# Optimization experiments

Hardware: AMD Instinct MI355X
Metric: run time of the kernel (lower is better)

The kernel has to match this reference:

```python
import jax, jax.numpy as jnp
import numpy as np

N = 10000        # nodes
E = 160000       # edges (avg degree 16)
MUL = 16         # multiplicity of each irrep in node features: '16x0e + 16x1o'
DIM_IN = 4 * MUL # 16 scalars + 16 vectors(3) = 64
DIM_SH = 4       # '1x0e + 1x1o' spherical harmonics
EMB = 18         # 2*4 (type embeds) + 10 (distance embed)
HID = 256
WNUM = 4 * MUL * MUL  # 4 tensor-product paths, 16x16 weights each


def setup_inputs() -> dict:
    key = jax.random.key(0)
    ks = jax.random.split(key, 8)
    node_features = jax.random.normal(ks[0], (N, DIM_IN), jnp.float32)
    edge_src = jax.random.randint(ks[1], (E,), 0, N, dtype=jnp.int32)
    edge_dst = jax.random.randint(ks[2], (E,), 0, N, dtype=jnp.int32)
    edge_attr = jax.random.normal(ks[3], (E, DIM_SH), jnp.float32)
    edge_embedding = jax.random.normal(ks[4], (E, EMB), jnp.float32)
    W1 = jax.random.normal(ks[5], (EMB, HID), jnp.float32) / np.sqrt(EMB)
    b1 = jnp.zeros((HID,), jnp.float32)
    W2 = jax.random.normal(ks[6], (HID, WNUM), jnp.float32) / np.sqrt(HID)
    b2 = jnp.zeros((WNUM,), jnp.float32)
    return dict(node_features=node_features, edge_attr=edge_attr,
                edge_embedding=edge_embedding, W1=W1, b1=b1, W2=W2, b2=b2,
                edge_src=edge_src, edge_dst=edge_dst)


def reference(node_features, edge_attr, edge_embedding, W1, b1, W2, b2, edge_src, edge_dst):
    # ---- edge MLP generates per-edge tensor-product weights ----
    h = jax.nn.silu(edge_embedding @ W1 + b1)          # [E, HID]
    w = (h @ W2 + b2).reshape(E, 4, MUL, MUL)          # [E, 4, 16, 16]
    w_ss, w_vv, w_sv, w_vs = w[:, 0], w[:, 1], w[:, 2], w[:, 3]

    # ---- gather source node features, split into irreps ----
    x = node_features[edge_src]                        # [E, 64]
    s = x[:, :MUL]                                     # [E, 16]   16x0e
    v = x[:, MUL:].reshape(E, MUL, 3)                  # [E, 16, 3] 16x1o
    y0 = edge_attr[:, 0]                               # [E]       1x0e sh
    y1 = edge_attr[:, 1:4]                             # [E, 3]    1x1o sh

    # ---- weighted Clebsch-Gordan tensor product (lmax=1 paths) ----
    inv_sqrt3 = np.float32(1.0 / np.sqrt(3.0))         # w3j(1,1,0), w3j(0,1,1), w3j(1,0,1)
    c_s = np.float32(np.sqrt(1.0 / (2 * MUL)))         # path norm: 2 paths, fan_in MUL each, out dim 1
    c_v = np.float32(np.sqrt(3.0 / (2 * MUL)))         # path norm: 2 paths, fan_in MUL each, out dim 3
    # 0e x 0e -> 0e  and  1o x 1o -> 0e
    out_s = c_s * (jnp.einsum('eij,e,ei->ej', w_ss, y0, s)
                   + inv_sqrt3 * jnp.einsum('eij,ea,eia->ej', w_vv, y1, v))   # [E, 16]
    # 0e x 1o -> 1o  and  1o x 0e -> 1o
    out_v = (c_v * inv_sqrt3) * (jnp.einsum('eij,ei,ea->eja', w_sv, s, y1)
                                 + jnp.einsum('eij,eia,e->eja', w_vs, v, y0))  # [E, 16, 3]

    edge_features = jnp.concatenate([out_s, out_v.reshape(E, 3 * MUL)], axis=1)  # [E, 64]

    # ---- scatter-reduce to destination nodes, normalized by sqrt(avg degree) ----
    num_neighbors = E / float(N)
    out = jax.ops.segment_sum(edge_features, edge_dst, num_segments=N)
    return out / np.float32(np.sqrt(num_neighbors))
```

## Files before the change

kernel.cpp:

```cpp
#include <hip/hip_runtime.h>
#include <math.h>


typedef __attribute__((ext_vector_type(8))) short s8v;
typedef __attribute__((ext_vector_type(4))) float f4v;
typedef unsigned short ushort_t;
typedef unsigned int uint_t;

#define NTHR 256
#define TE 64

__device__ __forceinline__ ushort_t f2bf(float x) {
    uint_t u = __float_as_uint(x);
    u += 0x7fffu + ((u >> 16) & 1u);
    return (ushort_t)(u >> 16);
}
__device__ __forceinline__ float bf2f(ushort_t v) {
    return __uint_as_float((uint_t)v << 16);
}

__global__ void prep_kernel(const float* __restrict__ W2, ushort_t* __restrict__ W2bf,
                            const int* __restrict__ edst, int* __restrict__ counts, int E) {
    if (blockIdx.x < 256) {
        int idx = blockIdx.x * 256 + threadIdx.x;
        int n  = idx & 1023;
        int k4 = (idx >> 10) << 2;
        uint_t lo = (uint_t)f2bf(W2[(size_t)(k4 + 0) * 1024 + n]) |
                    ((uint_t)f2bf(W2[(size_t)(k4 + 1) * 1024 + n]) << 16);
        uint_t hi = (uint_t)f2bf(W2[(size_t)(k4 + 2) * 1024 + n]) |
                    ((uint_t)f2bf(W2[(size_t)(k4 + 3) * 1024 + n]) << 16);
        ((uint2*)W2bf)[(n * 256 + k4) >> 2] = make_uint2(lo, hi);
    } else {
        int i = (blockIdx.x - 256) * 256 + threadIdx.x;
        if (i < E) atomicAdd(&counts[edst[i]], 1);
    }
}

__global__ __launch_bounds__(1024)
void scan_kernel(const int* __restrict__ counts, int* __restrict__ offsets, int N) {
    __shared__ int sdata[1024];
    const int t = threadIdx.x;
    const int C = (N + 1023) / 1024;
    const int lo = t * C;
    const int hi = min(lo + C, N);
    int sum = 0;
    for (int i = lo; i < hi; ++i) sum += counts[i];
    sdata[t] = sum;
    __syncthreads();
    for (int s = 1; s < 1024; s <<= 1) {
        int v = (t >= s) ? sdata[t - s] : 0;
        __syncthreads();
        sdata[t] += v;
        __syncthreads();
    }
    int run = sdata[t] - sum;
    for (int i = lo; i < hi; ++i) { offsets[i] = run; run += counts[i]; }
    if (t == 1023) offsets[N] = run;
}

__global__ __launch_bounds__(256)
void gather_kernel(const ushort_t* __restrict__ F,
                   const int* __restrict__ offsets,
                   const int* __restrict__ elist,
                   float* __restrict__ out, int N) {
    const int lane = threadIdx.x & 63;
    const int node = (blockIdx.x * 256 + threadIdx.x) >> 6;
    if (node >= N) return;
    const int base = offsets[node];
    const int end  = offsets[node + 1];
    float acc = 0.f;
    for (int j0 = base; j0 < end; j0 += 64) {
        const int rem = min(64, end - j0);
        int myeid = (lane < rem) ? elist[j0 + lane] : 0;
        int j = 0;
        for (; j + 4 <= rem; j += 4) {
            const int a0 = __shfl(myeid, j    );
            const int a1 = __shfl(myeid, j + 1);
            const int a2 = __shfl(myeid, j + 2);
            const int a3 = __shfl(myeid, j + 3);
            const float r0 = bf2f(F[(size_t)a0 * 64 + lane]);
            const float r1 = bf2f(F[(size_t)a1 * 64 + lane]);
            const float r2 = bf2f(F[(size_t)a2 * 64 + lane]);
            const float r3 = bf2f(F[(size_t)a3 * 64 + lane]);
            acc += (r0 + r1) + (r2 + r3);
        }
        for (; j < rem; ++j) {
            const int a = __shfl(myeid, j);
            acc += bf2f(F[(size_t)a * 64 + lane]);
        }
    }
    out[(size_t)node * 64 + lane] = acc;
}

__global__ __launch_bounds__(NTHR, 2)
void nequip_mfma(const float* __restrict__ nodef,
                 const float* __restrict__ eattr,
                 const float* __restrict__ eemb,
                 const float* __restrict__ W1,
                 const float* __restrict__ b1,
                 const ushort_t* __restrict__ W2bf,
                 const float* __restrict__ b2,
                 const int* __restrict__ esrc,
                 const int* __restrict__ edst,
                 const int* __restrict__ offs,
                 int* __restrict__ cursor,
                 int* __restrict__ elist,
                 ushort_t* __restrict__ F,
                 int E, float CC)
{
    __shared__ __align__(16) ushort_t sAu[TE * 256];
    __shared__ __align__(16) float sB2[1024];
    __shared__ __align__(16) float sEmb[TE * 18];
    __shared__ __align__(16) float sCss[16 * 64];
    __shared__ __align__(16) float sCvv[16 * 64];
    __shared__ __align__(16) float sCsv[16 * 64];
    __shared__ __align__(16) float sCvs[48 * 64];
    __shared__ __align__(16) float sAttrT[4 * 64];
    __shared__ __align__(16) float resSS[64 * 16];
    __shared__ __align__(16) float resSV[64 * 16];

    const int t  = threadIdx.x;
    const int e0 = blockIdx.x * TE;

    ((float4*)sB2)[t] = ((const float4*)b2)[t];
    for (int idx = t; idx < TE * 18; idx += NTHR) {
        size_t g = (size_t)e0 * 18 + idx;
        sEmb[idx] = (g < (size_t)E * 18) ? eemb[g] : 0.f;
    }
    if (t < TE) {
        int ge = e0 + t;
        float4 a = make_float4(0.f, 0.f, 0.f, 0.f);
        if (ge < E) {
            a = *(const float4*)(eattr + (size_t)ge * 4);
            const int d = edst[ge];
            const int pos = offs[d] + atomicAdd(&cursor[d], 1);
            elist[pos] = ge;
        }
        sAttrT[0 * 64 + t] = a.x; sAttrT[1 * 64 + t] = a.y;
        sAttrT[2 * 64 + t] = a.z; sAttrT[3 * 64 + t] = a.w;
    }
    {
        const int e = t >> 2, iq = t & 3;
        const int ge = e0 + e;
        const bool ok = ge < E;
        float y0 = 0.f, y1x = 0.f, y1y = 0.f, y1z = 0.f;
        int src = 0;
        if (ok) {
            float4 a = *(const float4*)(eattr + (size_t)ge * 4);
            y0 = a.x; y1x = a.y; y1y = a.z; y1z = a.w;
            src = esrc[ge];
        }
        const float* xp = nodef + (size_t)src * 64;
        float4 z = make_float4(0.f, 0.f, 0.f, 0.f);
        float4 sv = ok ? *(const float4*)(xp + iq * 4) : z;
        float4 v0 = ok ? *(const float4*)(xp + 16 + iq * 12) : z;
        float4 v1 = ok ? *(const float4*)(xp + 16 + iq * 12 + 4) : z;
        float4 v2 = ok ? *(const float4*)(xp + 16 + iq * 12 + 8) : z;
        const float K3 = CC * 0.57735026918962576f;
        float sarr[4] = { sv.x, sv.y, sv.z, sv.w };
        float varr[12] = { v0.x, v0.y, v0.z, v0.w, v1.x, v1.y, v1.z, v1.w,
                           v2.x, v2.y, v2.z, v2.w };
        #pragma unroll
        for (int j = 0; j < 4; ++j) {
            const int i = iq * 4 + j;
            const float s  = sarr[j];
            const float vx = varr[j * 3 + 0], vy = varr[j * 3 + 1], vz = varr[j * 3 + 2];
            sCss[i * 64 + e] = CC * y0 * s;
            sCvv[i * 64 + e] = K3 * (y1x * vx + y1y * vy + y1z * vz);
            sCsv[i * 64 + e] = CC * s;
            sCvs[(i * 3 + 0) * 64 + e] = CC * y0 * vx;
            sCvs[(i * 3 + 1) * 64 + e] = CC * y0 * vy;
            sCvs[(i * 3 + 2) * 64 + e] = CC * y0 * vz;
        }
    }
    __syncthreads();

    {
        const int p = t & 127;
        const int ehalf = t >> 7;
        const int n0 = 2 * p;
        float w1a[18], w1b[18];
        #pragma unroll
        for (int m = 0; m < 18; ++m) {
            float2 wv = *(const float2*)(W1 + m * 256 + n0);
            w1a[m] = wv.x; w1b[m] = wv.y;
        }
        const float2 bv = *(const float2*)(b1 + n0);
        const int kk = p >> 4;
        const int lhi = 16 * ((p >> 2) & 3);
        const int wsub = p & 3;
        uint_t* sA32 = (uint_t*)sAu;
        for (int er = 0; er < 32; ++er) {
            const int e = ehalf * 32 + er;
            float a0 = bv.x, a1 = bv.y;
            const float* ep = sEmb + e * 18;
            #pragma unroll
            for (int m = 0; m < 18; ++m) {
                const float em = ep[m];
                a0 = fmaf(em, w1a[m], a0);
                a1 = fmaf(em, w1b[m], a1);
            }
            a0 = a0 / (1.f + __expf(-a0));
            a1 = a1 / (1.f + __expf(-a1));
            const uint_t pk = (uint_t)f2bf(a0) | ((uint_t)f2bf(a1) << 16);
            const int lane_sw = ((e & 15) + lhi) ^ kk;
            sA32[(((e >> 4) * 8 + kk) * 64 + lane_sw) * 4 + wsub] = pk;
        }
    }
    __syncthreads();

    const int lane = t & 63;
    const int slab = t >> 6;
    const int jj   = lane & 15;
    const int q4   = lane >> 4;

    const ushort_t* Bl = W2bf + (size_t)jj * 256 + q4 * 8;

    float pS[4][4] = {{0.f}};
    float pV[3][4][4] = {{{0.f}}};

    if (slab < 3) {
        const float* C = (slab == 0) ? sCss : (slab == 1) ? sCvv : sCsv;
        #pragma unroll 1
        for (int g = 0; g < 8; ++g) {
            const int nb0 = slab * 256 + (2 * g) * 16;
            const int nb1 = nb0 + 16;
            f4v accA[4], accB[4];
            {
                const float bz0 = sB2[nb0 + jj];
                const float bz1 = sB2[nb1 + jj];
                #pragma unroll
                for (int mt = 0; mt < 4; ++mt) {
                    f4v zA; zA[0] = bz0; zA[1] = bz0; zA[2] = bz0; zA[3] = bz0;
                    f4v zB; zB[0] = bz1; zB[1] = bz1; zB[2] = bz1; zB[3] = bz1;
                    accA[mt] = zA; accB[mt] = zB;
                }
            }
            #pragma unroll
            for (int kk = 0; kk < 8; ++kk) {
                const s8v b0 = *(const s8v*)(Bl + (size_t)nb0 * 256 + kk * 32);
                const s8v b1 = *(const s8v*)(Bl + (size_t)nb1 * 256 + kk * 32);
                #pragma unroll
                for (int mt = 0; mt < 4; ++mt) {
                    const s8v a = *(const s8v*)(sAu + ((mt * 8 + kk) * 64 + (lane ^ kk)) * 8);
                    accA[mt] = __builtin_amdgcn_mfma_f32_16x16x32_bf16(a, b0, accA[mt], 0, 0, 0);
                    accB[mt] = __builtin_amdgcn_mfma_f32_16x16x32_bf16(a, b1, accB[mt], 0, 0, 0);
                }
            }
            const int i0 = 2 * g, i1 = 2 * g + 1;
            #pragma unroll
            for (int mt = 0; mt < 4; ++mt) {
                const int ebase = mt * 16 + q4 * 4;
                const float4 c0 = *(const float4*)(C + i0 * 64 + ebase);
                const float4 c1 = *(const float4*)(C + i1 * 64 + ebase);
                pS[mt][0] += c0.x * accA[mt][0] + c1.x * accB[mt][0];
                pS[mt][1] += c0.y * accA[mt][1] + c1.y * accB[mt][1];
                pS[mt][2] += c0.z * accA[mt][2] + c1.z * accB[mt][2];
                pS[mt][3] += c0.w * accA[mt][3] + c1.w * accB[mt][3];
            }
        }
        if (slab == 0) {
            #pragma unroll
            for (int mt = 0; mt < 4; ++mt)
                #pragma unroll
                for (int q = 0; q < 4; ++q)
                    resSS[(mt * 16 + q4 * 4 + q) * 16 + jj] = pS[mt][q];
        } else if (slab == 2) {
            #pragma unroll
            for (int mt = 0; mt < 4; ++mt)
                #pragma unroll
                for (int q = 0; q < 4; ++q)
                    resSV[(mt * 16 + q4 * 4 + q) * 16 + jj] = pS[mt][q];
        }
    } else {
        #pragma unroll
        for (int half = 0; half < 2; ++half) {
            #pragma unroll 1
            for (int g = 0; g < 8; ++g) {
                const int i0 = 2 * g, i1 = 2 * g + 1;
                const int nb0 = 3 * 256 + i0 * 16;
                const int nb1 = nb0 + 16;
                f4v acc0[2], acc1[2];
                {
                    const float bz0 = sB2[nb0 + jj];
                    const float bz1 = sB2[nb1 + jj];
                    #pragma unroll
                    for (int mt = 0; mt < 2; ++mt) {
                        f4v z0; z0[0] = bz0; z0[1] = bz0; z0[2] = bz0; z0[3] = bz0;
                        f4v z1; z1[0] = bz1; z1[1] = bz1; z1[2] = bz1; z1[3] = bz1;
                        acc0[mt] = z0; acc1[mt] = z1;
                    }
                }
                #pragma unroll
                for (int kk = 0; kk < 8; ++kk) {
                    const s8v b0 = *(const s8v*)(Bl + (size_t)nb0 * 256 + kk * 32);
                    const s8v b1 = *(const s8v*)(Bl + (size_t)nb1 * 256 + kk * 32);
                    #pragma unroll
                    for (int mt = 0; mt < 2; ++mt) {
                        const int mtg = half * 2 + mt;
                        const s8v a = *(const s8v*)(sAu + ((mtg * 8 + kk) * 64 + (lane ^ kk)) * 8);
                        acc0[mt] = __builtin_amdgcn_mfma_f32_16x16x32_bf16(a, b0, acc0[mt], 0, 0, 0);
                        acc1[mt] = __builtin_amdgcn_mfma_f32_16x16x32_bf16(a, b1, acc1[mt], 0, 0, 0);
                    }
                }
                #pragma unroll
                for (int mt = 0; mt < 2; ++mt) {
                    const int mtg = half * 2 + mt;
                    const int ebase = mtg * 16 + q4 * 4;
                    #pragma unroll
                    for (int a = 0; a < 3; ++a) {
                        const float4 c0 = *(const float4*)(sCvs + (i0 * 3 + a) * 64 + ebase);
                        const float4 c1 = *(const float4*)(sCvs + (i1 * 3 + a) * 64 + ebase);
                        pV[a][mtg][0] += c0.x * acc0[mt][0] + c1.x * acc1[mt][0];
                        pV[a][mtg][1] += c0.y * acc0[mt][1] + c1.y * acc1[mt][1];
                        pV[a][mtg][2] += c0.z * acc0[mt][2] + c1.z * acc1[mt][2];
                        pV[a][mtg][3] += c0.w * acc0[mt][3] + c1.w * acc1[mt][3];
                    }
                }
            }
        }
    }
    __syncthreads();

    if (slab == 1) {
        #pragma unroll
        for (int mt = 0; mt < 4; ++mt) {
            #pragma unroll
            for (int q = 0; q < 4; ++q) {
                const int e = mt * 16 + q4 * 4 + q;
                const int ge = e0 + e;
                if (ge < E) F[(size_t)ge * 64 + jj] = f2bf(resSS[e * 16 + jj] + pS[mt][q]);
            }
        }
    } else if (slab == 3) {
        #pragma unroll
        for (int mt = 0; mt < 4; ++mt) {
            #pragma unroll
            for (int q = 0; q < 4; ++q) {
                const int e = mt * 16 + q4 * 4 + q;
                const int ge = e0 + e;
                const float sv = resSV[e * 16 + jj];
                if (ge < E) {
                    #pragma unroll
                    for (int a = 0; a < 3; ++a)
                        F[(size_t)ge * 64 + 16 + jj * 3 + a] =
                            f2bf(fmaf(sAttrT[(1 + a) * 64 + e], sv, pV[a][mt][q]));
                }
            }
        }
    }
}

extern "C" void kernel_launch(void* const* d_in, const int* in_sizes, int n_in,
                              void* d_out, int out_size, void* d_ws, size_t ws_size,
                              hipStream_t stream)
{
    const float* node_features = (const float*)d_in[0];
    const float* edge_attr     = (const float*)d_in[1];
    const float* edge_emb      = (const float*)d_in[2];
    const float* W1            = (const float*)d_in[3];
    const float* b1            = (const float*)d_in[4];
    const float* W2            = (const float*)d_in[5];
    const float* b2            = (const float*)d_in[6];
    const int*   edge_src      = (const int*)d_in[7];
    const int*   edge_dst      = (const int*)d_in[8];
    float*       out           = (float*)d_out;

    const int E = in_sizes[7];
    const int N = out_size / 64;
    const float num_neigh = (float)E / (float)N;
    const float CC = 0.17677669529663689f / sqrtf(num_neigh);

    char* ws = (char*)d_ws;
    size_t off = 0;
    auto alloc = [&](size_t bytes) { char* p = ws + off; off = (off + bytes + 255) & ~(size_t)255; return p; };
    ushort_t* W2bf   = (ushort_t*)alloc((size_t)1024 * 256 * 2);
    int*      counts = (int*)alloc((size_t)2 * N * 4);
    int*      cursor = counts + N;
    int*      offs   = (int*)alloc((size_t)(N + 1) * 4);
    int*      elist  = (int*)alloc((size_t)E * 4);
    ushort_t* F      = (ushort_t*)alloc((size_t)E * 64 * 2);
    (void)ws_size;

    hipMemsetAsync(counts, 0, (size_t)2 * N * 4, stream);

    const int histBlocks = (E + 255) / 256;
    prep_kernel<<<256 + histBlocks, 256, 0, stream>>>(W2, W2bf, edge_dst, counts, E);
    scan_kernel<<<1, 1024, 0, stream>>>(counts, offs, N);

    const int blocks = (E + TE - 1) / TE;
    nequip_mfma<<<blocks, NTHR, 0, stream>>>(
        node_features, edge_attr, edge_emb, W1, b1, W2bf, b2,
        edge_src, edge_dst, offs, cursor, elist, F, E, CC);

    gather_kernel<<<(N + 3) / 4, 256, 0, stream>>>(F, offs, elist, out, N);
}
```

Before: 341.1 us.

## Double-buffer W2 fragment loads across groups and unify slab MFMA loops

The per-group W2 B-fragment global loads are moved into register double buffers, so the next group's fragments are prefetched while the current group's MFMAs run. The vector slab no longer runs two halves of 2 M-tiles each and instead does all 4 M-tiles in one pass, which halves its B-fragment reloads. The shared embedding rows are padded to 20 floats so the first-layer MLP can read them with float4 loads. Holding 32 s8v registers raises register pressure, which may cause spills or lower occupancy at the 2-blocks launch bound.

```diff
diff --git a/kernel.cpp b/kernel.cpp
--- a/kernel.cpp
+++ b/kernel.cpp
@@ -92,6 +92,66 @@
     out[(size_t)node * 64 + lane] = acc;
 }
 
+#define PREFB(B0, B1, g_) { \
+    const size_t nbo0 = (size_t)(slab * 256 + (2 * (g_)) * 16) * 256; \
+    const size_t nbo1 = nbo0 + (size_t)16 * 256; \
+    _Pragma("unroll") \
+    for (int kk = 0; kk < 8; ++kk) { \
+        B0[kk] = *(const s8v*)(Bl + nbo0 + kk * 32); \
+        B1[kk] = *(const s8v*)(Bl + nbo1 + kk * 32); \
+    } }
+
+#define GBODY(g_, B0, B1) { \
+    const int nb0 = slab * 256 + (2 * (g_)) * 16; \
+    const int nb1 = nb0 + 16; \
+    f4v accA[4], accB[4]; \
+    { \
+        const float bz0 = sB2[nb0 + jj]; \
+        const float bz1 = sB2[nb1 + jj]; \
+        _Pragma("unroll") \
+        for (int mt = 0; mt < 4; ++mt) { \
+            f4v zA; zA[0] = bz0; zA[1] = bz0; zA[2] = bz0; zA[3] = bz0; \
+            f4v zB; zB[0] = bz1; zB[1] = bz1; zB[2] = bz1; zB[3] = bz1; \
+            accA[mt] = zA; accB[mt] = zB; \
+        } \
+    } \
+    _Pragma("unroll") \
+    for (int kk = 0; kk < 8; ++kk) { \
+        _Pragma("unroll") \
+        for (int mt = 0; mt < 4; ++mt) { \
+            const s8v afr = *(const s8v*)(sAu + ((mt * 8 + kk) * 64 + (lane ^ kk)) * 8); \
+            accA[mt] = __builtin_amdgcn_mfma_f32_16x16x32_bf16(afr, B0[kk], accA[mt], 0, 0, 0); \
+            accB[mt] = __builtin_amdgcn_mfma_f32_16x16x32_bf16(afr, B1[kk], accB[mt], 0, 0, 0); \
+        } \
+    } \
+    const int i0 = 2 * (g_), i1 = i0 + 1; \
+    if (slab < 3) { \
+        _Pragma("unroll") \
+        for (int mt = 0; mt < 4; ++mt) { \
+            const int ebase = mt * 16 + q4 * 4; \
+            const float4 c0 = *(const float4*)(Cp + i0 * 64 + ebase); \
+            const float4 c1 = *(const float4*)(Cp + i1 * 64 + ebase); \
+            pS[mt][0] += c0.x * accA[mt][0] + c1.x * accB[mt][0]; \
+            pS[mt][1] += c0.y * accA[mt][1] + c1.y * accB[mt][1]; \
+            pS[mt][2] += c0.z * accA[mt][2] + c1.z * accB[mt][2]; \
+            pS[mt][3] += c0.w * accA[mt][3] + c1.w * accB[mt][3]; \
+        } \
+    } else { \
+        _Pragma("unroll") \
+        for (int mt = 0; mt < 4; ++mt) { \
+            const int ebase = mt * 16 + q4 * 4; \
+            _Pragma("unroll") \
+            for (int a2 = 0; a2 < 3; ++a2) { \
+                const float4 c0 = *(const float4*)(sCvs + (i0 * 3 + a2) * 64 + ebase); \
+                const float4 c1 = *(const float4*)(sCvs + (i1 * 3 + a2) * 64 + ebase); \
+                pV[a2][mt][0] += c0.x * accA[mt][0] + c1.x * accB[mt][0]; \
+                pV[a2][mt][1] += c0.y * accA[mt][1] + c1.y * accB[mt][1]; \
+                pV[a2][mt][2] += c0.z * accA[mt][2] + c1.z * accB[mt][2]; \
+                pV[a2][mt][3] += c0.w * accA[mt][3] + c1.w * accB[mt][3]; \
+            } \
+        } \
+    } }
+
 __global__ __launch_bounds__(NTHR, 2)
 void nequip_mfma(const float* __restrict__ nodef,
                  const float* __restrict__ eattr,
@@ -110,7 +170,7 @@
 {
     __shared__ __align__(16) ushort_t sAu[TE * 256];
     __shared__ __align__(16) float sB2[1024];
-    __shared__ __align__(16) float sEmb[TE * 18];
+    __shared__ __align__(16) float sEmb[TE * 20];
     __shared__ __align__(16) float sCss[16 * 64];
     __shared__ __align__(16) float sCvv[16 * 64];
     __shared__ __align__(16) float sCsv[16 * 64];
@@ -124,8 +184,10 @@
 
     ((float4*)sB2)[t] = ((const float4*)b2)[t];
     for (int idx = t; idx < TE * 18; idx += NTHR) {
+        const int e = idx / 18;
+        const int m = idx - e * 18;
         size_t g = (size_t)e0 * 18 + idx;
-        sEmb[idx] = (g < (size_t)E * 18) ? eemb[g] : 0.f;
+        sEmb[e * 20 + m] = (g < (size_t)E * 18) ? eemb[g] : 0.f;
     }
     if (t < TE) {
         int ge = e0 + t;
@@ -193,12 +255,21 @@
         for (int er = 0; er < 32; ++er) {
             const int e = ehalf * 32 + er;
             float a0 = bv.x, a1 = bv.y;
-            const float* ep = sEmb + e * 18;
+            const float* ep = sEmb + e * 20;
+            const float4 q0 = *(const float4*)(ep);
+            const float4 q1 = *(const float4*)(ep + 4);
+            const float4 q2 = *(const float4*)(ep + 8);
+            const float4 q3 = *(const float4*)(ep + 12);
+            const float2 q4v = *(const float2*)(ep + 16);
+            const float em[18] = { q0.x, q0.y, q0.z, q0.w,
+                                   q1.x, q1.y, q1.z, q1.w,
+                                   q2.x, q2.y, q2.z, q2.w,
+                                   q3.x, q3.y, q3.z, q3.w,
+                                   q4v.x, q4v.y };
             #pragma unroll
             for (int m = 0; m < 18; ++m) {
-                const float em = ep[m];
-                a0 = fmaf(em, w1a[m], a0);
-                a1 = fmaf(em, w1b[m], a1);
+                a0 = fmaf(em[m], w1a[m], a0);
+                a1 = fmaf(em[m], w1b[m], a1);
             }
             a0 = a0 / (1.f + __expf(-a0));
             a1 = a1 / (1.f + __expf(-a1));
@@ -215,110 +286,36 @@
     const int q4   = lane >> 4;
 
     const ushort_t* Bl = W2bf + (size_t)jj * 256 + q4 * 8;
+    const float* Cp = (slab == 0) ? sCss : (slab == 1) ? sCvv : sCsv;
 
     float pS[4][4] = {{0.f}};
     float pV[3][4][4] = {{{0.f}}};
 
-    if (slab < 3) {
-        const float* C = (slab == 0) ? sCss : (slab == 1) ? sCvv : sCsv;
+    {
+        s8v bX0[8], bX1[8], bY0[8], bY1[8];
+        PREFB(bX0, bX1, 0);
         #pragma unroll 1
-        for (int g = 0; g < 8; ++g) {
-            const int nb0 = slab * 256 + (2 * g) * 16;
-            const int nb1 = nb0 + 16;
-            f4v accA[4], accB[4];
-            {
-                const float bz0 = sB2[nb0 + jj];
-                const float bz1 = sB2[nb1 + jj];
-                #pragma unroll
-                for (int mt = 0; mt < 4; ++mt) {
-                    f4v zA; zA[0] = bz0; zA[1] = bz0; zA[2] = bz0; zA[3] = bz0;
-                    f4v zB; zB[0] = bz1; zB[1] = bz1; zB[2] = bz1; zB[3] = bz1;
-                    accA[mt] = zA; accB[mt] = zB;
-                }
-            }
-            #pragma unroll
-            for (int kk = 0; kk < 8; ++kk) {
-                const s8v b0 = *(const s8v*)(Bl + (size_t)nb0 * 256 + kk * 32);
-                const s8v b1 = *(const s8v*)(Bl + (size_t)nb1 * 256 + kk * 32);
-                #pragma unroll
-                for (int mt = 0; mt < 4; ++mt) {
-                    const s8v a = *(const s8v*)(sAu + ((mt * 8 + kk) * 64 + (lane ^ kk)) * 8);
-                    accA[mt] = __builtin_amdgcn_mfma_f32_16x16x32_bf16(a, b0, accA[mt], 0, 0, 0);
-                    accB[mt] = __builtin_amdgcn_mfma_f32_16x16x32_bf16(a, b1, accB[mt], 0, 0, 0);
-                }
-            }
-            const int i0 = 2 * g, i1 = 2 * g + 1;
-            #pragma unroll
-            for (int mt = 0; mt < 4; ++mt) {
-                const int ebase = mt * 16 + q4 * 4;
-                const float4 c0 = *(const float4*)(C + i0 * 64 + ebase);
-                const float4 c1 = *(const float4*)(C + i1 * 64 + ebase);
-                pS[mt][0] += c0.x * accA[mt][0] + c1.x * accB[mt][0];
-                pS[mt][1] += c0.y * accA[mt][1] + c1.y * accB[mt][1];
-                pS[mt][2] += c0.z * accA[mt][2] + c1.z * accB[mt][2];
-                pS[mt][3] += c0.w * accA[mt][3] + c1.w * accB[mt][3];
-            }
-        }
-        if (slab == 0) {
-            #pragma unroll
-            for (int mt = 0; mt < 4; ++mt)
-                #pragma unroll
-                for (int q = 0; q < 4; ++q)
-                    resSS[(mt * 16 + q4 * 4 + q) * 16 + jj] = pS[mt][q];
-        } else if (slab == 2) {
-            #pragma unroll
-            for (int mt = 0; mt < 4; ++mt)
-                #pragma unroll
-                for (int q = 0; q < 4; ++q)
-                    resSV[(mt * 16 + q4 * 4 + q) * 16 + jj] = pS[mt][q];
-        }
-    } else {
-        #pragma unroll
-        for (int half = 0; half < 2; ++half) {
-            #pragma unroll 1
-            for (int g = 0; g < 8; ++g) {
-                const int i0 = 2 * g, i1 = 2 * g + 1;
-                const int nb0 = 3 * 256 + i0 * 16;
-                const int nb1 = nb0 + 16;
-                f4v acc0[2], acc1[2];
-                {
-                    const float bz0 = sB2[nb0 + jj];
-                    const float bz1 = sB2[nb1 + jj];
-                    #pragma unroll
-                    for (int mt = 0; mt < 2; ++mt) {
-                        f4v z0; z0[0] = bz0; z0[1] = bz0; z0[2] = bz0; z0[3] = bz0;
-                        f4v z1; z1[0] = bz1; z1[1] = bz1; z1[2] = bz1; z1[3] = bz1;
-                        acc0[mt] = z0; acc1[mt] = z1;
-                    }
-                }
-                #pragma unroll
-                for (int kk = 0; kk < 8; ++kk) {
-                    const s8v b0 = *(const s8v*)(Bl + (size_t)nb0 * 256 + kk * 32);
-                    const s8v b1 = *(const s8v*)(Bl + (size_t)nb1 * 256 + kk * 32);
-                    #pragma unroll
-                    for (int mt = 0; mt < 2; ++mt) {
-                        const int mtg = half * 2 + mt;
-                        const s8v a = *(const s8v*)(sAu + ((mtg * 8 + kk) * 64 + (lane ^ kk)) * 8);
-                        acc0[mt] = __builtin_amdgcn_mfma_f32_16x16x32_bf16(a, b0, acc0[mt], 0, 0, 0);
-                        acc1[mt] = __builtin_amdgcn_mfma_f32_16x16x32_bf16(a, b1, acc1[mt], 0, 0, 0);
-                    }
-                }
-                #pragma unroll
-                for (int mt = 0; mt < 2; ++mt) {
-                    const int mtg = half * 2 + mt;
-                    const int ebase = mtg * 16 + q4 * 4;
-                    #pragma unroll
-                    for (int a = 0; a < 3; ++a) {
-                        const float4 c0 = *(const float4*)(sCvs + (i0 * 3 + a) * 64 + ebase);
-                        const float4 c1 = *(const float4*)(sCvs + (i1 * 3 + a) * 64 + ebase);
-                        pV[a][mtg][0] += c0.x * acc0[mt][0] + c1.x * acc1[mt][0];
-                        pV[a][mtg][1] += c0.y * acc0[mt][1] + c1.y * acc1[mt][1];
-                        pV[a][mtg][2] += c0.z * acc0[mt][2] + c1.z * acc1[mt][2];
-                        pV[a][mtg][3] += c0.w * acc0[mt][3] + c1.w * acc1[mt][3];
-                    }
-                }
-            }
-        }
+        for (int g2 = 0; g2 < 4; ++g2) {
+            const int ga = 2 * g2, gb = 2 * g2 + 1;
+            PREFB(bY0, bY1, gb);
+            GBODY(ga, bX0, bX1);
+            if (g2 < 3) PREFB(bX0, bX1, gb + 1);
+            GBODY(gb, bY0, bY1);
+        }
+    }
+
+    if (slab == 0) {
+        #pragma unroll
+        for (int mt = 0; mt < 4; ++mt)
+            #pragma unroll
+            for (int q = 0; q < 4; ++q)
+                resSS[(mt * 16 + q4 * 4 + q) * 16 + jj] = pS[mt][q];
+    } else if (slab == 2) {
+        #pragma unroll
+        for (int mt = 0; mt < 4; ++mt)
+            #pragma unroll
+            for (int q = 0; q < 4; ++q)
+                resSV[(mt * 16 + q4 * 4 + q) * 16 + jj] = pS[mt][q];
     }
     __syncthreads();
 
```

Measured after the change: 620.7 us. 1.82x slower.

## Switch edge-weight GEMM to 32x32x16 MFMA tiles with shuffle reduction

Applied to the files above, without the earlier changes.

Replaces the 16x16x32 bf16 MFMA tiling of the per-edge weight GEMM with 32x32x16 MFMA tiles, which changes the accumulator layout and how lanes map to edges and output columns. Each 32-column tile now mixes two i-index groups, and the partial sums from the two lane halves are combined with xor-16 shuffles. The aim is fewer MFMA instructions and fewer LDS/global operand loads per FLOP. In exchange, each lane holds more accumulator registers (16-wide vectors and larger pS/pV arrays), which may reduce occupancy, and the index remapping is intricate enough to risk correctness errors.

```diff
diff --git a/kernel.cpp b/kernel.cpp
--- a/kernel.cpp
+++ b/kernel.cpp
@@ -3,7 +3,7 @@
 
 
 typedef __attribute__((ext_vector_type(8))) short s8v;
-typedef __attribute__((ext_vector_type(4))) float f4v;
+typedef __attribute__((ext_vector_type(16))) float f16v;
 typedef unsigned short ushort_t;
 typedef unsigned int uint_t;
 
@@ -211,140 +211,168 @@
 
     const int lane = t & 63;
     const int slab = t >> 6;
-    const int jj   = lane & 15;
-    const int q4   = lane >> 4;
-
-    const ushort_t* Bl = W2bf + (size_t)jj * 256 + q4 * 8;
-
-    float pS[4][4] = {{0.f}};
-    float pV[3][4][4] = {{{0.f}}};
+    const int lo16 = lane & 15;
+    const int ip   = (lane >> 4) & 1;
+    const int lh   = lane >> 5;
+    const int col  = lane & 31;
+
+    float pS[2][16] = {{0.f}};
+    float pV[3][2][16] = {{{0.f}}};
 
     if (slab < 3) {
         const float* C = (slab == 0) ? sCss : (slab == 1) ? sCvv : sCsv;
         #pragma unroll 1
+        for (int g = 0; g < 4; ++g) {
+            const int n0 = slab * 256 + (2 * g) * 32;
+            const ushort_t* Bp0 = W2bf + (size_t)(n0 + col) * 256 + lh * 8;
+            const ushort_t* Bp1 = Bp0 + (size_t)32 * 256;
+            f16v c00, c01, c10, c11;
+            {
+                const float bz0 = sB2[n0 + col];
+                const float bz1 = sB2[n0 + 32 + col];
+                #pragma unroll
+                for (int r = 0; r < 16; ++r) { c00[r] = bz0; c01[r] = bz1; c10[r] = bz0; c11[r] = bz1; }
+            }
+            #pragma unroll
+            for (int ks = 0; ks < 16; ++ks) {
+                const int kk16 = ks >> 1;
+                const int lsw = (lo16 + 32 * (ks & 1) + 16 * lh) ^ kk16;
+                const s8v a0 = *(const s8v*)(sAu + (((0 + ip) * 8 + kk16) * 64 + lsw) * 8);
+                const s8v a1 = *(const s8v*)(sAu + (((2 + ip) * 8 + kk16) * 64 + lsw) * 8);
+                const s8v b0 = *(const s8v*)(Bp0 + ks * 16);
+                const s8v b1 = *(const s8v*)(Bp1 + ks * 16);
+                c00 = __builtin_amdgcn_mfma_f32_32x32x16_bf16(a0, b0, c00, 0, 0, 0);
+                c01 = __builtin_amdgcn_mfma_f32_32x32x16_bf16(a0, b1, c01, 0, 0, 0);
+                c10 = __builtin_amdgcn_mfma_f32_32x32x16_bf16(a1, b0, c10, 0, 0, 0);
+                c11 = __builtin_amdgcn_mfma_f32_32x32x16_bf16(a1, b1, c11, 0, 0, 0);
+            }
+            const float* Ci0 = C + (4 * g + ip) * 64 + 4 * lh;
+            const float* Ci1 = C + (4 * g + 2 + ip) * 64 + 4 * lh;
+            #pragma unroll
+            for (int q = 0; q < 4; ++q) {
+                const float4 cA0 = *(const float4*)(Ci0 + 8 * q);
+                const float4 cA1 = *(const float4*)(Ci0 + 32 + 8 * q);
+                const float4 cB0 = *(const float4*)(Ci1 + 8 * q);
+                const float4 cB1 = *(const float4*)(Ci1 + 32 + 8 * q);
+                pS[0][4*q+0] += cA0.x * c00[4*q+0] + cB0.x * c01[4*q+0];
+                pS[0][4*q+1] += cA0.y * c00[4*q+1] + cB0.y * c01[4*q+1];
+                pS[0][4*q+2] += cA0.z * c00[4*q+2] + cB0.z * c01[4*q+2];
+                pS[0][4*q+3] += cA0.w * c00[4*q+3] + cB0.w * c01[4*q+3];
+                pS[1][4*q+0] += cA1.x * c10[4*q+0] + cB1.x * c11[4*q+0];
+                pS[1][4*q+1] += cA1.y * c10[4*q+1] + cB1.y * c11[4*q+1];
+                pS[1][4*q+2] += cA1.z * c10[4*q+2] + cB1.z * c11[4*q+2];
+                pS[1][4*q+3] += cA1.w * c10[4*q+3] + cB1.w * c11[4*q+3];
+            }
+        }
+        #pragma unroll
+        for (int mt = 0; mt < 2; ++mt)
+            #pragma unroll
+            for (int r = 0; r < 16; ++r)
+                pS[mt][r] += __shfl_xor(pS[mt][r], 16);
+    } else {
+        #pragma unroll 1
         for (int g = 0; g < 8; ++g) {
-            const int nb0 = slab * 256 + (2 * g) * 16;
-            const int nb1 = nb0 + 16;
-            f4v accA[4], accB[4];
+            const int n0 = 3 * 256 + g * 32;
+            const ushort_t* Bp = W2bf + (size_t)(n0 + col) * 256 + lh * 8;
+            f16v c0, c1;
             {
-                const float bz0 = sB2[nb0 + jj];
-                const float bz1 = sB2[nb1 + jj];
+                const float bz = sB2[n0 + col];
                 #pragma unroll
-                for (int mt = 0; mt < 4; ++mt) {
-                    f4v zA; zA[0] = bz0; zA[1] = bz0; zA[2] = bz0; zA[3] = bz0;
-                    f4v zB; zB[0] = bz1; zB[1] = bz1; zB[2] = bz1; zB[3] = bz1;
-                    accA[mt] = zA; accB[mt] = zB;
+                for (int r = 0; r < 16; ++r) { c0[r] = bz; c1[r] = bz; }
+            }
+            #pragma unroll
+            for (int ks = 0; ks < 16; ++ks) {
+                const int kk16 = ks >> 1;
+                const int lsw = (lo16 + 32 * (ks & 1) + 16 * lh) ^ kk16;
+                const s8v a0 = *(const s8v*)(sAu + (((0 + ip) * 8 + kk16) * 64 + lsw) * 8);
+                const s8v a1 = *(const s8v*)(sAu + (((2 + ip) * 8 + kk16) * 64 + lsw) * 8);
+                const s8v b  = *(const s8v*)(Bp + ks * 16);
+                c0 = __builtin_amdgcn_mfma_f32_32x32x16_bf16(a0, b, c0, 0, 0, 0);
+                c1 = __builtin_amdgcn_mfma_f32_32x32x16_bf16(a1, b, c1, 0, 0, 0);
+            }
+            const int ib = (2 * g + ip) * 3;
+            #pragma unroll
+            for (int a = 0; a < 3; ++a) {
+                const float* Cv = sCvs + (ib + a) * 64 + 4 * lh;
+                #pragma unroll
+                for (int q = 0; q < 4; ++q) {
+                    const float4 c0f = *(const float4*)(Cv + 8 * q);
+                    const float4 c1f = *(const float4*)(Cv + 32 + 8 * q);
+                    pV[a][0][4*q+0] += c0f.x * c0[4*q+0];
+                    pV[a][0][4*q+1] += c0f.y * c0[4*q+1];
+                    pV[a][0][4*q+2] += c0f.z * c0[4*q+2];
+                    pV[a][0][4*q+3] += c0f.w * c0[4*q+3];
+                    pV[a][1][4*q+0] += c1f.x * c1[4*q+0];
+                    pV[a][1][4*q+1] += c1f.y * c1[4*q+1];
+                    pV[a][1][4*q+2] += c1f.z * c1[4*q+2];
+                    pV[a][1][4*q+3] += c1f.w * c1[4*q+3];
                 }
             }
-            #pragma unroll
-            for (int kk = 0; kk < 8; ++kk) {
-                const s8v b0 = *(const s8v*)(Bl + (size_t)nb0 * 256 + kk * 32);
-                const s8v b1 = *(const s8v*)(Bl + (size_t)nb1 * 256 + kk * 32);
+        }
+        #pragma unroll
+        for (int a = 0; a < 3; ++a)
+            #pragma unroll
+            for (int mt = 0; mt < 2; ++mt)
                 #pragma unroll
-                for (int mt = 0; mt < 4; ++mt) {
-                    const s8v a = *(const s8v*)(sAu + ((mt * 8 + kk) * 64 + (lane ^ kk)) * 8);
-                    accA[mt] = __builtin_amdgcn_mfma_f32_16x16x32_bf16(a, b0, accA[mt], 0, 0, 0);
-                    accB[mt] = __builtin_amdgcn_mfma_f32_16x16x32_bf16(a, b1, accB[mt], 0, 0, 0);
-                }
-            }
-            const int i0 = 2 * g, i1 = 2 * g + 1;
-            #pragma unroll
-            for (int mt = 0; mt < 4; ++mt) {
-                const int ebase = mt * 16 + q4 * 4;
-                const float4 c0 = *(const float4*)(C + i0 * 64 + ebase);
-                const float4 c1 = *(const float4*)(C + i1 * 64 + ebase);
-                pS[mt][0] += c0.x * accA[mt][0] + c1.x * accB[mt][0];
-                pS[mt][1] += c0.y * accA[mt][1] + c1.y * accB[mt][1];
-                pS[mt][2] += c0.z * accA[mt][2] + c1.z * accB[mt][2];
-                pS[mt][3] += c0.w * accA[mt][3] + c1.w * accB[mt][3];
-            }
-        }
-        if (slab == 0) {
-            #pragma unroll
-            for (int mt = 0; mt < 4; ++mt)
-                #pragma unroll
-                for (int q = 0; q < 4; ++q)
-                    resSS[(mt * 16 + q4 * 4 + q) * 16 + jj] = pS[mt][q];
-        } else if (slab == 2) {
-            #pragma unroll
-            for (int mt = 0; mt < 4; ++mt)
-                #pragma unroll
-                for (int q = 0; q < 4; ++q)
-                    resSV[(mt * 16 + q4 * 4 + q) * 16 + jj] = pS[mt][q];
-        }
-    } else {
-        #pragma unroll
-        for (int half = 0; half < 2; ++half) {
-            #pragma unroll 1
-            for (int g = 0; g < 8; ++g) {
-                const int i0 = 2 * g, i1 = 2 * g + 1;
-                const int nb0 = 3 * 256 + i0 * 16;
-                const int nb1 = nb0 + 16;
-                f4v acc0[2], acc1[2];
-                {
-                    const float bz0 = sB2[nb0 + jj];
-                    const float bz1 = sB2[nb1 + jj];
-                    #pragma unroll
-                    for (int mt = 0; mt < 2; ++mt) {
-                        f4v z0; z0[0] = bz0; z0[1] = bz0; z0[2] = bz0; z0[3] = bz0;
-                        f4v z1; z1[0] = bz1; z1[1] = bz1; z1[2] = bz1; z1[3] = bz1;
-                        acc0[mt] = z0; acc1[mt] = z1;
-                    }
-                }
-                #pragma unroll
-                for (int kk = 0; kk < 8; ++kk) {
-                    const s8v b0 = *(const s8v*)(Bl + (size_t)nb0 * 256 + kk * 32);
-                    const s8v b1 = *(const s8v*)(Bl + (size_t)nb1 * 256 + kk * 32);
-                    #pragma unroll
-                    for (int mt = 0; mt < 2; ++mt) {
-                        const int mtg = half * 2 + mt;
-                        const s8v a = *(const s8v*)(sAu + ((mtg * 8 + kk) * 64 + (lane ^ kk)) * 8);
-                        acc0[mt] = __builtin_amdgcn_mfma_f32_16x16x32_bf16(a, b0, acc0[mt], 0, 0, 0);
-                        acc1[mt] = __builtin_amdgcn_mfma_f32_16x16x32_bf16(a, b1, acc1[mt], 0, 0, 0);
-                    }
-                }
-                #pragma unroll
-                for (int mt = 0; mt < 2; ++mt) {
-                    const int mtg = half * 2 + mt;
-                    const int ebase = mtg * 16 + q4 * 4;
-                    #pragma unroll
-                    for (int a = 0; a < 3; ++a) {
-                        const float4 c0 = *(const float4*)(sCvs + (i0 * 3 + a) * 64 + ebase);
-                        const float4 c1 = *(const float4*)(sCvs + (i1 * 3 + a) * 64 + ebase);
-                        pV[a][mtg][0] += c0.x * acc0[mt][0] + c1.x * acc1[mt][0];
-                        pV[a][mtg][1] += c0.y * acc0[mt][1] + c1.y * acc1[mt][1];
-                        pV[a][mtg][2] += c0.z * acc0[mt][2] + c1.z * acc1[mt][2];
-                        pV[a][mtg][3] += c0.w * acc0[mt][3] + c1.w * acc1[mt][3];
-                    }
-                }
-            }
+                for (int r = 0; r < 16; ++r)
+                    pV[a][mt][r] += __shfl_xor(pV[a][mt][r], 16);
+    }
+
+    if (slab == 0 || slab == 2) {
+        float* res = (slab == 0) ? resSS : resSV;
+        if (ip == 0) {
+            #pragma unroll
+            for (int r = 0; r < 16; ++r)
+                res[(4 * lh + 8 * (r >> 2) + (r & 3)) * 16 + lo16] = pS[0][r];
+        } else {
+            #pragma unroll
+            for (int r = 0; r < 16; ++r)
+                res[(32 + 4 * lh + 8 * (r >> 2) + (r & 3)) * 16 + lo16] = pS[1][r];
         }
     }
     __syncthreads();
 
     if (slab == 1) {
-        #pragma unroll
-        for (int mt = 0; mt < 4; ++mt) {
-            #pragma unroll
-            for (int q = 0; q < 4; ++q) {
-                const int e = mt * 16 + q4 * 4 + q;
+        if (ip == 0) {
+            #pragma unroll
+            for (int r = 0; r < 16; ++r) {
+                const int e = 4 * lh + 8 * (r >> 2) + (r & 3);
                 const int ge = e0 + e;
-                if (ge < E) F[(size_t)ge * 64 + jj] = f2bf(resSS[e * 16 + jj] + pS[mt][q]);
+                if (ge < E) F[(size_t)ge * 64 + lo16] = f2bf(resSS[e * 16 + lo16] + pS[0][r]);
+            }
+        } else {
+            #pragma unroll
+            for (int r = 0; r < 16; ++r) {
+                const int e = 32 + 4 * lh + 8 * (r >> 2) + (r & 3);
+                const int ge = e0 + e;
+                if (ge < E) F[(size_t)ge * 64 + lo16] = f2bf(resSS[e * 16 + lo16] + pS[1][r]);
             }
         }
     } else if (slab == 3) {
-        #pragma unroll
-        for (int mt = 0; mt < 4; ++mt) {
-            #pragma unroll
-            for (int q = 0; q < 4; ++q) {
-                const int e = mt * 16 + q4 * 4 + q;
+        if (ip == 0) {
+            #pragma unroll
+            for (int r = 0; r < 16; ++r) {
+                const int e = 4 * lh + 8 * (r >> 2) + (r & 3);
                 const int ge = e0 + e;
-                const float sv = resSV[e * 16 + jj];
+                const float sv = resSV[e * 16 + lo16];
                 if (ge < E) {
                     #pragma unroll
                     for (int a = 0; a < 3; ++a)
-                        F[(size_t)ge * 64 + 16 + jj * 3 + a] =
-                            f2bf(fmaf(sAttrT[(1 + a) * 64 + e], sv, pV[a][mt][q]));
+                        F[(size_t)ge * 64 + 16 + lo16 * 3 + a] =
+                            f2bf(fmaf(sAttrT[(1 + a) * 64 + e], sv, pV[a][0][r]));
+                }
+            }
+        } else {
+            #pragma unroll
+            for (int r = 0; r < 16; ++r) {
+                const int e = 32 + 4 * lh + 8 * (r >> 2) + (r & 3);
+                const int ge = e0 + e;
+                const float sv = resSV[e * 16 + lo16];
+                if (ge < E) {
+                    #pragma unroll
+                    for (int a = 0; a < 3; ++a)
+                        F[(size_t)ge * 64 + 16 + lo16 * 3 + a] =
+                            f2bf(fmaf(sAttrT[(1 + a) * 64 + e], sv, pV[a][1][r]));
                 }
             }
         }
```

After: 412.3 us. +20.9%, slower.
